# Kernel optimization log

Measured on AMD Instinct MI355X. Metric: run time of the kernel, lower is better.

The kernel has to match this reference:

```python
import jax, jax.numpy as jnp
import numpy as np

N = 100000      # nodes
D = 64          # feature dim (in_channels == out_channels)
K = 16          # num_neighbors -> E = N*(K-1) directed edges
NEG_SLOPE = 0.2 # GATConv negative_slope


def setup_inputs() -> dict:
    key = jax.random.key(0)
    k1, k2, k3, k4, k5 = jax.random.split(key, 5)
    E = N * (K - 1)
    x = jax.random.normal(k1, (N, D), dtype=jnp.float32)
    edge_index = jax.random.randint(k2, (2, E), 0, N, dtype=jnp.int32)
    W = jax.random.normal(k3, (D, D), dtype=jnp.float32) / np.sqrt(D).astype(np.float32)
    att_src = jax.random.normal(k4, (D,), dtype=jnp.float32) / np.sqrt(D).astype(np.float32)
    att_dst = jax.random.normal(k5, (D,), dtype=jnp.float32) / np.sqrt(D).astype(np.float32)
    bias = jnp.zeros((D,), dtype=jnp.float32)
    return {"x": x, "edge_index": edge_index, "W": W,
            "att_src": att_src, "att_dst": att_dst, "bias": bias}


def gat_forward(x, W, att_src, att_dst, bias, src, dst):
    # PyG GATConv, heads=1, concat=True, dropout=0, + outer ReLU from LNLE.forward
    h = x @ W                                   # [N, D] transformed nodes
    a_src = h @ att_src                         # [N] source attention logits
    a_dst = h @ att_dst                         # [N] target attention logits
    e = jax.nn.leaky_relu(a_src[src] + a_dst[dst], NEG_SLOPE)  # [E]
    # numerically-stable segment softmax over edges grouped by destination
    emax = jax.ops.segment_max(e, dst, num_segments=N)         # [N]
    p = jnp.exp(e - emax[dst])                                 # [E]
    psum = jax.ops.segment_sum(p, dst, num_segments=N)         # [N]
    alpha = p / (psum[dst] + jnp.float32(1e-16))               # [E]
    msg = h[src] * alpha[:, None]                              # [E, D] gather + weight
    out = jax.ops.segment_sum(msg, dst, num_segments=N) + bias # [N, D] scatter-add
    return jax.nn.relu(out)


def reference(x, edge_index, W, att_src, att_dst, bias):
    # GATConv default add_self_loops=True: append (i -> i) for every node
    loops = jnp.arange(N, dtype=edge_index.dtype)
    src = jnp.concatenate([edge_index[0], loops])   # message sources j
    dst = jnp.concatenate([edge_index[1], loops])   # message targets i
    return gat_forward(x, W, att_src, att_dst, bias, src, dst)
```

## Files before the change

kernel.cpp:

```cpp
#include <hip/hip_runtime.h>
#include <hip/hip_bf16.h>
#include <hip/hip_fp16.h>


#define GAT_N 100000
#define GAT_D 64
#define GAT_E 1500000
#define NEG_SLOPE 0.2f
#define NB ((GAT_N + 255) >> 8)
#define PC 3072
#define CAP_P 5120
#define CAP_C (CAP_P + 256)
#define RPAD 16
#define GPITCH 68
#define GEMM_BLKS ((GAT_N + 63) / 64)
#define PART_BLKS ((GAT_E + PC - 1) / PC)

__device__ __forceinline__ float lrelu(float e) {
    return e > 0.f ? e : NEG_SLOPE * e;
}

__global__ __launch_bounds__(256) void zinit_k(int* __restrict__ runctr) {
    const int i = blockIdx.x * 256 + threadIdx.x;
    if (i < NB) runctr[i * RPAD] = i * CAP_P;
}

__global__ __launch_bounds__(256, 4) void pg_k(
        const float* __restrict__ x, const float* __restrict__ W,
        const float* __restrict__ att_s, const float* __restrict__ att_d,
        unsigned* __restrict__ h, float* __restrict__ a_src, float* __restrict__ a_dst,
        const int* __restrict__ src, const int* __restrict__ dst,
        int* __restrict__ runctr, int* __restrict__ pairs) {
    __shared__ __align__(16) int smem[8448];
    const int t = threadIdx.x;

    if (blockIdx.x < GEMM_BLKS) {
        float* xl = (float*)smem;
        float* Wl = (float*)(smem + 4352);
        const int rowbase = blockIdx.x * 64;
        {
            const float4* W4 = (const float4*)W;
            float4* Wl4 = (float4*)Wl;
            #pragma unroll
            for (int i = 0; i < 4; ++i) Wl4[i * 256 + t] = W4[i * 256 + t];
        }
        #pragma unroll
        for (int i = 0; i < 4; ++i) {
            const int g = i * 256 + t;
            const int row = g >> 4, c4 = g & 15;
            float4 v = make_float4(0.f, 0.f, 0.f, 0.f);
            if (rowbase + row < GAT_N)
                v = ((const float4*)x)[(size_t)(rowbase + row) * 16 + c4];
            *(float4*)&xl[row * GPITCH + c4 * 4] = v;
        }
        __syncthreads();

        const int tx = t & 15, ty = t >> 4;
        float4 acc[4] = {};
        #pragma unroll 4
        for (int k0 = 0; k0 < GAT_D; k0 += 4) {
            const float4 w0 = *(const float4*)&Wl[(k0 + 0) * 64 + tx * 4];
            const float4 w1 = *(const float4*)&Wl[(k0 + 1) * 64 + tx * 4];
            const float4 w2 = *(const float4*)&Wl[(k0 + 2) * 64 + tx * 4];
            const float4 w3 = *(const float4*)&Wl[(k0 + 3) * 64 + tx * 4];
            #pragma unroll
            for (int i = 0; i < 4; ++i) {
                const float4 xv = *(const float4*)&xl[(ty * 4 + i) * GPITCH + k0];
                acc[i].x = fmaf(xv.x, w0.x, fmaf(xv.y, w1.x, fmaf(xv.z, w2.x, fmaf(xv.w, w3.x, acc[i].x))));
                acc[i].y = fmaf(xv.x, w0.y, fmaf(xv.y, w1.y, fmaf(xv.z, w2.y, fmaf(xv.w, w3.y, acc[i].y))));
                acc[i].z = fmaf(xv.x, w0.z, fmaf(xv.y, w1.z, fmaf(xv.z, w2.z, fmaf(xv.w, w3.z, acc[i].z))));
                acc[i].w = fmaf(xv.x, w0.w, fmaf(xv.y, w1.w, fmaf(xv.z, w2.w, fmaf(xv.w, w3.w, acc[i].w))));
            }
        }
        const float4 as4 = ((const float4*)att_s)[tx];
        const float4 ad4 = ((const float4*)att_d)[tx];
        #pragma unroll
        for (int i = 0; i < 4; ++i) {
            const int row = rowbase + ty * 4 + i;
            if (row < GAT_N) {
                const __half2 lo = __floats2half2_rn(acc[i].x, acc[i].y);
                const __half2 hi = __floats2half2_rn(acc[i].z, acc[i].w);
                ((uint2*)h)[(size_t)row * 16 + tx] =
                    make_uint2(*(const unsigned*)&lo, *(const unsigned*)&hi);
            }
            float ps = acc[i].x * as4.x + acc[i].y * as4.y + acc[i].z * as4.z + acc[i].w * as4.w;
            float pd = acc[i].x * ad4.x + acc[i].y * ad4.y + acc[i].z * ad4.z + acc[i].w * ad4.w;
            #pragma unroll
            for (int o = 8; o > 0; o >>= 1) {
                ps += __shfl_down(ps, o, 64);
                pd += __shfl_down(pd, o, 64);
            }
            if (tx == 0 && row < GAT_N) { a_src[row] = ps; a_dst[row] = pd; }
        }
    } else {
        int* lh    = smem;
        int* sc    = smem + 512;
        int* lb    = smem + 768;
        int* gpos  = smem + 1280;
        int* run   = smem + 1792;
        int* tgt   = smem + 2304;
        int* stage = smem + 5376;
        const int base = (blockIdx.x - GEMM_BLKS) * PC;

        lh[t] = 0; lh[t + 256] = 0;
        __syncthreads();
        for (int i = t; i < PC; i += 256) {
            const int e = base + i;
            if (e < GAT_E) atomicAdd(&lh[dst[e] >> 8], 1);
        }
        __syncthreads();
        const int a = lh[2 * t], b = lh[2 * t + 1];
        sc[t] = a + b; __syncthreads();
        for (int off = 1; off < 256; off <<= 1) {
            const int xch = (t >= off) ? sc[t - off] : 0;
            __syncthreads();
            sc[t] += xch;
            __syncthreads();
        }
        const int base0 = sc[t] - (a + b);
        lb[2 * t] = base0; lb[2 * t + 1] = base0 + a;
        #pragma unroll
        for (int k = 0; k < 2; ++k) {
            const int i = 2 * t + k;
            run[i] = lb[i];
            gpos[i] = (i < NB && lh[i]) ? atomicAdd(&runctr[i * RPAD], lh[i]) : 0;
        }
        __syncthreads();
        for (int i = t; i < PC; i += 256) {
            const int e = base + i;
            if (e < GAT_E) {
                const int sv = src[e], dv = dst[e];
                const int bk = dv >> 8;
                const int slot = atomicAdd(&run[bk], 1);
                stage[slot] = (sv << 8) | (dv & 255);
                tgt[slot] = gpos[bk] + (slot - lb[bk]);
            }
        }
        __syncthreads();
        const int cnt_total = min(PC, GAT_E - base);
        for (int i = t; i < cnt_total; i += 256) pairs[tgt[i]] = stage[i];
    }
}

__global__ __launch_bounds__(512) void csr_bucket_k(
        const int* __restrict__ pairs, const int* __restrict__ runctr,
        int* __restrict__ rowinfo, int* __restrict__ csr) {
    __shared__ int cnt[256], pfx[256];
    __shared__ int lcsr[CAP_C];
    const int b = blockIdx.x;
    const int t = threadIdx.x;
    const int node0 = b << 8;
    const int nnodes = min(256, GAT_N - node0);
    const int pbeg = b * CAP_P;
    const int ne = runctr[b * RPAD] - pbeg;
    const int cbase = b * CAP_C;

    if (t < 256) cnt[t] = (t < nnodes) ? 1 : 0;
    __syncthreads();
    for (int i = t; i < ne; i += 512)
        atomicAdd(&cnt[pairs[pbeg + i] & 255], 1);
    __syncthreads();
    if (t < 256) pfx[t] = cnt[t];
    __syncthreads();
    for (int off = 1; off < 256; off <<= 1) {
        const int x = (t < 256 && t >= off) ? pfx[t - off] : 0;
        __syncthreads();
        if (t < 256) pfx[t] += x;
        __syncthreads();
    }
    if (t < 256) {
        const int v = cnt[t];
        const int excl = pfx[t] - v;
        if (t < nnodes) {
            rowinfo[node0 + t] = ((cbase + excl) << 8) | v;
            lcsr[excl] = node0 + t;
        }
        cnt[t] = excl + ((t < nnodes) ? 1 : 0);
    }
    __syncthreads();
    for (int i = t; i < ne; i += 512) {
        const int p = pairs[pbeg + i];
        const int pos = atomicAdd(&cnt[p & 255], 1);
        lcsr[pos] = p >> 8;
    }
    __syncthreads();
    const int tot = ne + nnodes;
    for (int i = t; i < tot; i += 512) csr[cbase + i] = lcsr[i];
}

#define GATHER4(ACC, EIDX)                                              \
    {                                                                   \
        const float w_ = __shfl(alpha, (EIDX), 64);                     \
        const int   s_ = __shfl(s, (EIDX), 64);                         \
        const uint2 v_ = h2[(size_t)s_ * 16 + fl];                      \
        const float2 fa_ = __half22float2(*(const __half2*)&v_.x);      \
        const float2 fb_ = __half22float2(*(const __half2*)&v_.y);      \
        ACC.x = fmaf(w_, fa_.x, ACC.x);                                 \
        ACC.y = fmaf(w_, fa_.y, ACC.y);                                 \
        ACC.z = fmaf(w_, fb_.x, ACC.z);                                 \
        ACC.w = fmaf(w_, fb_.y, ACC.w);                                 \
    }

__device__ __noinline__ void gat_one_node(
        int d, int beg, int deg, int lane,
        const int* __restrict__ csr_src,
        const float* __restrict__ a_src, const float* __restrict__ a_dst,
        const unsigned* __restrict__ h, const float* __restrict__ bias,
        float* __restrict__ out) {
    const int end = beg + deg;
    const float ad = a_dst[d];
    if (deg <= 64) {
        const int k = beg + lane;
        const bool valid = k < end;
        const int s = valid ? csr_src[k] : 0;
        const float e = valid ? lrelu(a_src[s] + ad) : -3.4e38f;
        float m = e;
        #pragma unroll
        for (int o = 32; o > 0; o >>= 1) m = fmaxf(m, __shfl_down(m, o, 64));
        m = __shfl(m, 0, 64);
        const float p = valid ? __expf(e - m) : 0.f;
        float S = p;
        #pragma unroll
        for (int o = 32; o > 0; o >>= 1) S += __shfl_down(S, o, 64);
        S = __shfl(S, 0, 64);
        const float alpha = p / (S + 1e-16f);
        const int q = lane >> 4, fl = lane & 15;
        const uint2* __restrict__ h2 = (const uint2*)h;
        float4 A = {0,0,0,0}, B = {0,0,0,0}, C = {0,0,0,0}, D = {0,0,0,0};
        int j = 0;
        for (; j + 16 <= deg; j += 16) {
            GATHER4(A, j + q);
            GATHER4(B, j + 4 + q);
            GATHER4(C, j + 8 + q);
            GATHER4(D, j + 12 + q);
        }
        if (j < deg)      GATHER4(A, j + q);
        if (j + 4 < deg)  GATHER4(B, j + 4 + q);
        if (j + 8 < deg)  GATHER4(C, j + 8 + q);
        if (j + 12 < deg) GATHER4(D, j + 12 + q);
        float4 acc;
        acc.x = (A.x + B.x) + (C.x + D.x);
        acc.y = (A.y + B.y) + (C.y + D.y);
        acc.z = (A.z + B.z) + (C.z + D.z);
        acc.w = (A.w + B.w) + (C.w + D.w);
        acc.x += __shfl_xor(acc.x, 16, 64); acc.x += __shfl_xor(acc.x, 32, 64);
        acc.y += __shfl_xor(acc.y, 16, 64); acc.y += __shfl_xor(acc.y, 32, 64);
        acc.z += __shfl_xor(acc.z, 16, 64); acc.z += __shfl_xor(acc.z, 32, 64);
        acc.w += __shfl_xor(acc.w, 16, 64); acc.w += __shfl_xor(acc.w, 32, 64);
        if (q == 0) {
            const float4 bi = ((const float4*)bias)[fl];
            float4 o;
            o.x = fmaxf(acc.x + bi.x, 0.f);
            o.y = fmaxf(acc.y + bi.y, 0.f);
            o.z = fmaxf(acc.z + bi.z, 0.f);
            o.w = fmaxf(acc.w + bi.w, 0.f);
            ((float4*)out)[(size_t)d * 16 + fl] = o;
        }
    } else {
        float m = -3.4e38f;
        for (int base = beg; base < end; base += 64) {
            const int k = base + lane;
            if (k < end) m = fmaxf(m, lrelu(a_src[csr_src[k]] + ad));
        }
        #pragma unroll
        for (int o = 32; o > 0; o >>= 1) m = fmaxf(m, __shfl_down(m, o, 64));
        m = __shfl(m, 0, 64);
        float S = 0.f;
        for (int base = beg; base < end; base += 64) {
            const int k = base + lane;
            if (k < end) S += __expf(lrelu(a_src[csr_src[k]] + ad) - m);
        }
        #pragma unroll
        for (int o = 32; o > 0; o >>= 1) S += __shfl_down(S, o, 64);
        S = __shfl(S, 0, 64);
        const float inv = 1.f / (S + 1e-16f);
        float acc = 0.f;
        const unsigned short* hb = (const unsigned short*)h;
        for (int base = beg; base < end; base += 64) {
            const int k = base + lane;
            int s = 0; float alpha = 0.f;
            if (k < end) {
                s = csr_src[k];
                alpha = __expf(lrelu(a_src[s] + ad) - m) * inv;
            }
            const int lim = min(64, end - base);
            for (int j2 = 0; j2 < lim; ++j2) {
                const float aj = __shfl(alpha, j2, 64);
                const int   sj = __shfl(s, j2, 64);
                const unsigned short u = hb[(size_t)sj * 64 + lane];
                acc = fmaf(aj, __half2float(*(const __half*)&u), acc);
            }
        }
        const float v = acc + bias[lane];
        out[(size_t)d * GAT_D + lane] = v > 0.f ? v : 0.f;
    }
}

__global__ __launch_bounds__(256) void gat_node_k(
        const int* __restrict__ rowinfo, const int* __restrict__ csr_src,
        const float* __restrict__ a_src, const float* __restrict__ a_dst,
        const unsigned* __restrict__ h, const float* __restrict__ bias,
        float* __restrict__ out) {
    const int pair = blockIdx.x * 4 + (threadIdx.x >> 6);
    const int lane = threadIdx.x & 63;
    const int half = lane >> 5, l32 = lane & 31;
    const int n0 = pair * 2;
    const int n = n0 + half;

    const int ri  = rowinfo[n];
    const int beg = ri >> 8;
    const int deg = ri & 255;
    const int dm  = max(deg, __shfl_xor(deg, 32, 64));

    if (dm <= 31) {
        const float ad = a_dst[n];
        const bool valid = l32 < deg;
        const int k = beg + l32;
        const int s = valid ? csr_src[k] : 0;
        const float e0 = valid ? lrelu(a_src[s] + ad) : -3.4e38f;
        float m = e0;
        #pragma unroll
        for (int o = 16; o > 0; o >>= 1) m = fmaxf(m, __shfl_xor(m, o, 64));
        const float p = valid ? __expf(e0 - m) : 0.f;
        float S = p;
        #pragma unroll
        for (int o = 16; o > 0; o >>= 1) S += __shfl_xor(S, o, 64);
        const float alpha = p / (S + 1e-16f);

        const int g = l32 >> 3, f = l32 & 7;
        const int hb5 = lane & 32;
        const uint4* __restrict__ h4 = (const uint4*)h;
        float4 aL = {0,0,0,0}, aH = {0,0,0,0};
        #pragma unroll
        for (int i = 0; i < 8; ++i) {
            const int sl = hb5 + i * 4 + g;
            const float w_ = __shfl(alpha, sl, 64);
            const int   s_ = __shfl(s,     sl, 64);
            const uint4 v_ = h4[(size_t)s_ * 8 + f];
            const float2 f0 = __half22float2(*(const __half2*)&v_.x);
            const float2 f1 = __half22float2(*(const __half2*)&v_.y);
            const float2 f2 = __half22float2(*(const __half2*)&v_.z);
            const float2 f3 = __half22float2(*(const __half2*)&v_.w);
            aL.x = fmaf(w_, f0.x, aL.x); aL.y = fmaf(w_, f0.y, aL.y);
            aL.z = fmaf(w_, f1.x, aL.z); aL.w = fmaf(w_, f1.y, aL.w);
            aH.x = fmaf(w_, f2.x, aH.x); aH.y = fmaf(w_, f2.y, aH.y);
            aH.z = fmaf(w_, f3.x, aH.z); aH.w = fmaf(w_, f3.y, aH.w);
        }
        #pragma unroll
        for (int o = 8; o <= 16; o <<= 1) {
            aL.x += __shfl_xor(aL.x, o, 64); aL.y += __shfl_xor(aL.y, o, 64);
            aL.z += __shfl_xor(aL.z, o, 64); aL.w += __shfl_xor(aL.w, o, 64);
            aH.x += __shfl_xor(aH.x, o, 64); aH.y += __shfl_xor(aH.y, o, 64);
            aH.z += __shfl_xor(aH.z, o, 64); aH.w += __shfl_xor(aH.w, o, 64);
        }
        if (g == 0) {
            const float4 bL = ((const float4*)bias)[2 * f];
            const float4 bH = ((const float4*)bias)[2 * f + 1];
            float4 oL, oH;
            oL.x = fmaxf(aL.x + bL.x, 0.f);
            oL.y = fmaxf(aL.y + bL.y, 0.f);
            oL.z = fmaxf(aL.z + bL.z, 0.f);
            oL.w = fmaxf(aL.w + bL.w, 0.f);
            oH.x = fmaxf(aH.x + bH.x, 0.f);
            oH.y = fmaxf(aH.y + bH.y, 0.f);
            oH.z = fmaxf(aH.z + bH.z, 0.f);
            oH.w = fmaxf(aH.w + bH.w, 0.f);
            ((float4*)out)[(size_t)n * 16 + 2 * f]     = oL;
            ((float4*)out)[(size_t)n * 16 + 2 * f + 1] = oH;
        }
    } else {
        const int ri0 = rowinfo[n0];
        gat_one_node(n0, ri0 >> 8, ri0 & 255, lane, csr_src, a_src, a_dst, h, bias, out);
        const int ri1 = rowinfo[n0 + 1];
        gat_one_node(n0 + 1, ri1 >> 8, ri1 & 255, lane, csr_src, a_src, a_dst, h, bias, out);
    }
}

extern "C" void kernel_launch(void* const* d_in, const int* in_sizes, int n_in,
                              void* d_out, int out_size, void* d_ws, size_t ws_size,
                              hipStream_t stream) {
    const float* x     = (const float*)d_in[0];
    const int*   ei    = (const int*)  d_in[1];
    const float* W     = (const float*)d_in[2];
    const float* att_s = (const float*)d_in[3];
    const float* att_d = (const float*)d_in[4];
    const float* bias  = (const float*)d_in[5];
    float* out = (float*)d_out;

    unsigned* h      = (unsigned*)d_ws;
    float*  a_src    = (float*)(h + (size_t)GAT_N * 32);
    float*  a_dst    = a_src + GAT_N;
    int*    pairs    = (int*)(a_dst + GAT_N);
    int*    runctr   = pairs + (size_t)NB * CAP_P;
    int*    rowinfo  = runctr + (size_t)NB * RPAD;
    int*    csr      = rowinfo + GAT_N;

    const int* src = ei;
    const int* dst = ei + GAT_E;

    zinit_k<<<2, 256, 0, stream>>>(runctr);
    pg_k<<<GEMM_BLKS + PART_BLKS, 256, 0, stream>>>(
        x, W, att_s, att_d, h, a_src, a_dst, src, dst, runctr, pairs);
    csr_bucket_k<<<NB, 512, 0, stream>>>(pairs, runctr, rowinfo, csr);
    gat_node_k<<<GAT_N / 8, 256, 0, stream>>>(rowinfo, csr, a_src, a_dst, h, bias, out);
}
```

Measured before the change: 164.5 us.

## Split node GEMM across partition and CSR kernels, vectorize edge loads

```diff
diff --git a/kernel.cpp b/kernel.cpp
--- a/kernel.cpp
+++ b/kernel.cpp
@@ -14,6 +14,8 @@
 #define RPAD 16
 #define GPITCH 68
 #define GEMM_BLKS ((GAT_N + 63) / 64)
+#define G1 (GEMM_BLKS / 2)
+#define G2 (GEMM_BLKS - G1)
 #define PART_BLKS ((GAT_E + PC - 1) / PC)
 
 __device__ __forceinline__ float lrelu(float e) {
@@ -34,7 +36,7 @@
     __shared__ __align__(16) int smem[8448];
     const int t = threadIdx.x;
 
-    if (blockIdx.x < GEMM_BLKS) {
+    if (blockIdx.x < G1) {
         float* xl = (float*)smem;
         float* Wl = (float*)(smem + 4352);
         const int rowbase = blockIdx.x * 64;
@@ -100,13 +102,20 @@
         int* run   = smem + 1792;
         int* tgt   = smem + 2304;
         int* stage = smem + 5376;
-        const int base = (blockIdx.x - GEMM_BLKS) * PC;
+        const int base = (blockIdx.x - G1) * PC;
+        const int cnt_total = min(PC, GAT_E - base);
+        const int nv = cnt_total >> 2;
+        const int4* __restrict__ d4p = (const int4*)(dst + base);
+        const int4* __restrict__ s4p = (const int4*)(src + base);
 
         lh[t] = 0; lh[t + 256] = 0;
         __syncthreads();
-        for (int i = t; i < PC; i += 256) {
-            const int e = base + i;
-            if (e < GAT_E) atomicAdd(&lh[dst[e] >> 8], 1);
+        for (int i = t; i < nv; i += 256) {
+            const int4 d4 = d4p[i];
+            atomicAdd(&lh[d4.x >> 8], 1);
+            atomicAdd(&lh[d4.y >> 8], 1);
+            atomicAdd(&lh[d4.z >> 8], 1);
+            atomicAdd(&lh[d4.w >> 8], 1);
         }
         __syncthreads();
         const int a = lh[2 * t], b = lh[2 * t + 1];
@@ -126,66 +135,135 @@
             gpos[i] = (i < NB && lh[i]) ? atomicAdd(&runctr[i * RPAD], lh[i]) : 0;
         }
         __syncthreads();
-        for (int i = t; i < PC; i += 256) {
-            const int e = base + i;
-            if (e < GAT_E) {
-                const int sv = src[e], dv = dst[e];
-                const int bk = dv >> 8;
-                const int slot = atomicAdd(&run[bk], 1);
-                stage[slot] = (sv << 8) | (dv & 255);
-                tgt[slot] = gpos[bk] + (slot - lb[bk]);
-            }
-        }
-        __syncthreads();
-        const int cnt_total = min(PC, GAT_E - base);
+        for (int i = t; i < nv; i += 256) {
+            const int4 d4 = d4p[i];
+            const int4 s4 = s4p[i];
+            #define PART1(SV, DV)                                       \
+                {                                                       \
+                    const int bk_ = (DV) >> 8;                          \
+                    const int slot_ = atomicAdd(&run[bk_], 1);          \
+                    stage[slot_] = ((SV) << 8) | ((DV) & 255);          \
+                    tgt[slot_] = gpos[bk_] + (slot_ - lb[bk_]);         \
+                }
+            PART1(s4.x, d4.x) PART1(s4.y, d4.y)
+            PART1(s4.z, d4.z) PART1(s4.w, d4.w)
+            #undef PART1
+        }
+        __syncthreads();
         for (int i = t; i < cnt_total; i += 256) pairs[tgt[i]] = stage[i];
     }
 }
 
-__global__ __launch_bounds__(512) void csr_bucket_k(
+__global__ __launch_bounds__(512, 8) void cg_k(
+        const float* __restrict__ x, const float* __restrict__ W,
+        const float* __restrict__ att_s, const float* __restrict__ att_d,
+        unsigned* __restrict__ h, float* __restrict__ a_src, float* __restrict__ a_dst,
         const int* __restrict__ pairs, const int* __restrict__ runctr,
         int* __restrict__ rowinfo, int* __restrict__ csr) {
-    __shared__ int cnt[256], pfx[256];
-    __shared__ int lcsr[CAP_C];
-    const int b = blockIdx.x;
+    __shared__ __align__(16) int smem[8448];
     const int t = threadIdx.x;
-    const int node0 = b << 8;
-    const int nnodes = min(256, GAT_N - node0);
-    const int pbeg = b * CAP_P;
-    const int ne = runctr[b * RPAD] - pbeg;
-    const int cbase = b * CAP_C;
-
-    if (t < 256) cnt[t] = (t < nnodes) ? 1 : 0;
-    __syncthreads();
-    for (int i = t; i < ne; i += 512)
-        atomicAdd(&cnt[pairs[pbeg + i] & 255], 1);
-    __syncthreads();
-    if (t < 256) pfx[t] = cnt[t];
-    __syncthreads();
-    for (int off = 1; off < 256; off <<= 1) {
-        const int x = (t < 256 && t >= off) ? pfx[t - off] : 0;
-        __syncthreads();
-        if (t < 256) pfx[t] += x;
-        __syncthreads();
+
+    if (blockIdx.x < NB) {
+        int* cnt  = smem;
+        int* pfx  = smem + 256;
+        int* lcsr = smem + 512;
+        const int b = blockIdx.x;
+        const int node0 = b << 8;
+        const int nnodes = min(256, GAT_N - node0);
+        const int pbeg = b * CAP_P;
+        const int ne = runctr[b * RPAD] - pbeg;
+        const int cbase = b * CAP_C;
+
+        if (t < 256) cnt[t] = (t < nnodes) ? 1 : 0;
+        __syncthreads();
+        for (int i = t; i < ne; i += 512)
+            atomicAdd(&cnt[pairs[pbeg + i] & 255], 1);
+        __syncthreads();
+        if (t < 256) pfx[t] = cnt[t];
+        __syncthreads();
+        for (int off = 1; off < 256; off <<= 1) {
+            const int x2 = (t < 256 && t >= off) ? pfx[t - off] : 0;
+            __syncthreads();
+            if (t < 256) pfx[t] += x2;
+            __syncthreads();
+        }
+        if (t < 256) {
+            const int v = cnt[t];
+            const int excl = pfx[t] - v;
+            if (t < nnodes) {
+                rowinfo[node0 + t] = ((cbase + excl) << 8) | v;
+                lcsr[excl] = node0 + t;
+            }
+            cnt[t] = excl + ((t < nnodes) ? 1 : 0);
+        }
+        __syncthreads();
+        for (int i = t; i < ne; i += 512) {
+            const int p = pairs[pbeg + i];
+            const int pos = atomicAdd(&cnt[p & 255], 1);
+            lcsr[pos] = p >> 8;
+        }
+        __syncthreads();
+        const int tot = ne + nnodes;
+        for (int i = t; i < tot; i += 512) csr[cbase + i] = lcsr[i];
+    } else {
+        float* xl = (float*)smem;
+        float* Wl = (float*)(smem + 4352);
+        const int rowbase = (G1 + (blockIdx.x - NB)) * 64;
+        {
+            const float4* W4 = (const float4*)W;
+            float4* Wl4 = (float4*)Wl;
+            #pragma unroll
+            for (int i = 0; i < 2; ++i) Wl4[i * 512 + t] = W4[i * 512 + t];
+        }
+        #pragma unroll
+        for (int i = 0; i < 2; ++i) {
+            const int g = i * 512 + t;
+            const int row = g >> 4, c4 = g & 15;
+            float4 v = make_float4(0.f, 0.f, 0.f, 0.f);
+            if (rowbase + row < GAT_N)
+                v = ((const float4*)x)[(size_t)(rowbase + row) * 16 + c4];
+            *(float4*)&xl[row * GPITCH + c4 * 4] = v;
+        }
+        __syncthreads();
+
+        const int tx = t & 15, ty = t >> 4;
+        float4 acc[2] = {};
+        #pragma unroll 4
+        for (int k0 = 0; k0 < GAT_D; k0 += 4) {
+            const float4 w0 = *(const float4*)&Wl[(k0 + 0) * 64 + tx * 4];
+            const float4 w1 = *(const float4*)&Wl[(k0 + 1) * 64 + tx * 4];
+            const float4 w2 = *(const float4*)&Wl[(k0 + 2) * 64 + tx * 4];
+            const float4 w3 = *(const float4*)&Wl[(k0 + 3) * 64 + tx * 4];
+            #pragma unroll
+            for (int i = 0; i < 2; ++i) {
+                const float4 xv = *(const float4*)&xl[(ty * 2 + i) * GPITCH + k0];
+                acc[i].x = fmaf(xv.x, w0.x, fmaf(xv.y, w1.x, fmaf(xv.z, w2.x, fmaf(xv.w, w3.x, acc[i].x))));
+                acc[i].y = fmaf(xv.x, w0.y, fmaf(xv.y, w1.y, fmaf(xv.z, w2.y, fmaf(xv.w, w3.y, acc[i].y))));
+                acc[i].z = fmaf(xv.x, w0.z, fmaf(xv.y, w1.z, fmaf(xv.z, w2.z, fmaf(xv.w, w3.z, acc[i].z))));
+                acc[i].w = fmaf(xv.x, w0.w, fmaf(xv.y, w1.w, fmaf(xv.z, w2.w, fmaf(xv.w, w3.w, acc[i].w))));
+            }
+        }
+        const float4 as4 = ((const float4*)att_s)[tx];
+        const float4 ad4 = ((const float4*)att_d)[tx];
+        #pragma unroll
+        for (int i = 0; i < 2; ++i) {
+            const int row = rowbase + ty * 2 + i;
+            if (row < GAT_N) {
+                const __half2 lo = __floats2half2_rn(acc[i].x, acc[i].y);
+                const __half2 hi = __floats2half2_rn(acc[i].z, acc[i].w);
+                ((uint2*)h)[(size_t)row * 16 + tx] =
+                    make_uint2(*(const unsigned*)&lo, *(const unsigned*)&hi);
+            }
+            float ps = acc[i].x * as4.x + acc[i].y * as4.y + acc[i].z * as4.z + acc[i].w * as4.w;
+            float pd = acc[i].x * ad4.x + acc[i].y * ad4.y + acc[i].z * ad4.z + acc[i].w * ad4.w;
+            #pragma unroll
+            for (int o = 8; o > 0; o >>= 1) {
+                ps += __shfl_down(ps, o, 64);
+                pd += __shfl_down(pd, o, 64);
+            }
+            if (tx == 0 && row < GAT_N) { a_src[row] = ps; a_dst[row] = pd; }
+        }
     }
-    if (t < 256) {
-        const int v = cnt[t];
-        const int excl = pfx[t] - v;
-        if (t < nnodes) {
-            rowinfo[node0 + t] = ((cbase + excl) << 8) | v;
-            lcsr[excl] = node0 + t;
-        }
-        cnt[t] = excl + ((t < nnodes) ? 1 : 0);
-    }
-    __syncthreads();
-    for (int i = t; i < ne; i += 512) {
-        const int p = pairs[pbeg + i];
-        const int pos = atomicAdd(&cnt[p & 255], 1);
-        lcsr[pos] = p >> 8;
-    }
-    __syncthreads();
-    const int tot = ne + nnodes;
-    for (int i = t; i < tot; i += 512) csr[cbase + i] = lcsr[i];
 }
 
 #define GATHER4(ACC, EIDX)                                              \
@@ -399,8 +477,9 @@
     const int* dst = ei + GAT_E;
 
     zinit_k<<<2, 256, 0, stream>>>(runctr);
-    pg_k<<<GEMM_BLKS + PART_BLKS, 256, 0, stream>>>(
+    pg_k<<<G1 + PART_BLKS, 256, 0, stream>>>(
         x, W, att_s, att_d, h, a_src, a_dst, src, dst, runctr, pairs);
-    csr_bucket_k<<<NB, 512, 0, stream>>>(pairs, runctr, rowinfo, csr);
+    cg_k<<<NB + G2, 512, 0, stream>>>(
+        x, W, att_s, att_d, h, a_src, a_dst, pairs, runctr, rowinfo, csr);
     gat_node_k<<<GAT_N / 8, 256, 0, stream>>>(rowinfo, csr, a_src, a_dst, h, bias, out);
 }
```

Result: faster. 160.2 us (-2.6%).
